# Performance work log

Hardware: AMD Instinct MI355X
Metric: run time of the kernel (lower is better)

## Reference

```python
import jax, jax.numpy as jnp
import numpy as np

T, B, E, H = 2048, 2, 2048, 16
D = E // H  # 128


def setup_inputs() -> dict:
    key = jax.random.key(0)
    ks = jax.random.split(key, 4)
    query = jax.random.normal(ks[0], (T, B, E), dtype=jnp.float32)
    Wqkv = jax.random.normal(ks[1], (3 * E, E), dtype=jnp.float32) * 0.02
    bqkv = jnp.zeros((3 * E,), dtype=jnp.float32)
    Wo = jax.random.normal(ks[2], (E, E), dtype=jnp.float32) * 0.02
    bo = jnp.zeros((E,), dtype=jnp.float32)
    # Llama rotary frequencies: freqs_cis[t, j] = exp(i * t * theta^{-2j/D})
    inv_freq = 1.0 / (10000.0 ** (np.arange(0, D, 2, dtype=np.float32) / D))  # (D/2,)
    angles = np.arange(T, dtype=np.float32)[:, None] * inv_freq[None, :]       # (T, D/2)
    freqs_cos = jnp.asarray(np.cos(angles), dtype=jnp.float32)
    freqs_sin = jnp.asarray(np.sin(angles), dtype=jnp.float32)
    return {"query": query, "Wqkv": Wqkv, "bqkv": bqkv, "Wo": Wo, "bo": bo,
            "freqs_cos": freqs_cos, "freqs_sin": freqs_sin}


def _apply_rope(x, cos, sin):
    # Faithful to metaseq: x is (T, B, E) but view()-ed as (B, T, H, D);
    # jnp.reshape is the same row-major reinterpretation as torch .view().
    xr = x.reshape(B, T, H, D // 2, 2)
    x0, x1 = xr[..., 0], xr[..., 1]
    c = cos[None, :, None, :]  # broadcast over batch and heads, seq_dim=1
    s = sin[None, :, None, :]
    o0 = x0 * c - x1 * s
    o1 = x0 * s + x1 * c
    return jnp.stack([o0, o1], axis=-1).reshape(T, B, E)


def reference(query, Wqkv, bqkv, Wo, bo, freqs_cos, freqs_sin):
    # Combined QKV projection (ColumnParallelLinear, world_size=1), split order (k, v, q)
    kvq = jnp.einsum('tbe,fe->tbf', query, Wqkv) + bqkv  # (T, B, 3E)
    k, v, q = jnp.split(kvq, 3, axis=-1)
    q = _apply_rope(q, freqs_cos, freqs_sin)
    k = _apply_rope(k, freqs_cos, freqs_sin)
    # scaling split as sqrt(head_dim^-0.5) on both q and k (baddbmm path)
    s = jnp.asarray(D, jnp.float32) ** -0.25
    qb = q.reshape(T, B * H, D).swapaxes(0, 1) * s   # (BH, T, D)
    kb = k.reshape(T, B * H, D).swapaxes(0, 1) * s   # (BH, S, D)
    vb = v.reshape(T, B * H, D).swapaxes(0, 1)       # (BH, S, D)
    scores = jnp.einsum('btd,bsd->bts', qb, kb)      # (BH, T, S)
    causal = jnp.tril(jnp.ones((T, T), dtype=bool))  # ScaledUpperTriangMaskedSoftmax
    scores = jnp.where(causal[None, :, :], scores, jnp.finfo(scores.dtype).min)
    probs = jax.nn.softmax(scores, axis=-1)          # dropout p=0 -> identity
    attn = jnp.einsum('bts,bsd->btd', probs, vb)     # (BH, T, D)
    attn = attn.swapaxes(0, 1).reshape(T, B, E)
    # RowParallelLinear with skip_bias_add=True: bias returned separately (not added)
    out = jnp.einsum('tbe,fe->tbf', attn, Wo)
    return out
```

## Files before the change

kernel.cpp:

```cpp
#include <hip/hip_runtime.h>
#include <stdint.h>

typedef unsigned short u16;
typedef __attribute__((ext_vector_type(4))) float f32x4;
typedef __attribute__((ext_vector_type(8))) short bf16x8;
typedef __attribute__((ext_vector_type(8))) u16 u16x8;

#define T_SEQ  2048
#define EMB    2048
#define HD     128
#define NHEAD  16
#define NTOK   4096
#define NE3    6144
#define SCALE  0.29730177875068026f
#define LOG2E  1.44269504088896f

typedef __attribute__((address_space(3))) char* lds_t;
typedef const __attribute__((address_space(1))) char* gl_t;

__device__ __forceinline__ void gld16(const void* g, void* l) {
  __builtin_amdgcn_global_load_lds((gl_t)g, (lds_t)l, 16, 0, 0);
}

__device__ __forceinline__ u16 f2bf(float f) {
  union { float f; uint32_t u; } c; c.f = f;
  uint32_t r = c.u + 0x7fffu + ((c.u >> 16) & 1u);
  return (u16)(r >> 16);
}

__global__ __launch_bounds__(256) void cvt_bf16(const float* __restrict__ in,
                                                u16* __restrict__ out, int n8) {
  int i = blockIdx.x * 256 + threadIdx.x;
  if (i >= n8) return;
  const float4* p = (const float4*)in + (size_t)i * 2;
  float4 a = p[0], b = p[1];
  u16x8 o;
  o[0]=f2bf(a.x); o[1]=f2bf(a.y); o[2]=f2bf(a.z); o[3]=f2bf(a.w);
  o[4]=f2bf(b.x); o[5]=f2bf(b.y); o[6]=f2bf(b.z); o[7]=f2bf(b.w);
  *((u16x8*)out + i) = o;
}


__device__ __forceinline__ bf16x8 rdfrag(const char* slot, int row, int lq) {
  return *(const bf16x8*)(slot + row*64 + ((lq ^ ((row >> 1) & 3)) << 4));
}
__device__ __forceinline__ void stageA(const char* Ag, int K2, int ktb, int ks,
                                       char* slot, int tid) {
  int row = tid >> 2, c = tid & 3;
  gld16(Ag + (size_t)row*K2 + ktb + ks*64 + ((c ^ ((row >> 1) & 3)) << 4),
        slot + tid*16);
}
__device__ __forceinline__ void stageB(const char* Bg, int K2, int ktb, int ks,
                                       char* slot, int j, int tid) {
  int lb = j*8192 + tid*16;
  int row = lb >> 6, c = (lb >> 4) & 3;
  gld16(Bg + (size_t)row*K2 + ktb + ks*64 + ((c ^ ((row >> 1) & 3)) << 4),
        slot + lb);
}

template<int EPI, int NBN>
__global__ __launch_bounds__(512, 2) void gemmP(
    const u16* __restrict__ A, const u16* __restrict__ Bm, int K, int N,
    const float* __restrict__ cosT, const float* __restrict__ sinT,
    const float* __restrict__ bias,
    u16* __restrict__ Qh, u16* __restrict__ Kh, u16* __restrict__ Vt,
    float* __restrict__ Cout)
{
  __shared__ __align__(16) char lds[147456];
  const int tid = threadIdx.x;
  const int lane = tid & 63, w = tid >> 6;
  const int wm = w >> 2, wn = w & 3;
  const int l15 = lane & 15, lq = lane >> 4;

  const int i = blockIdx.x;
  const int r = i >> 8, x = i & 7, s = (i >> 3) & 31;
  const int regionId = r*8 + x;
  const int RM = regionId & 3, RN = regionId >> 2;
  const int bM = RM*8 + (s >> 2);
  const int bN = RN*4 + (s & 3);

  const char* Ag = (const char*)(A + (size_t)bM * 128 * K);
  const char* Bg = (const char*)(Bm + (size_t)bN * 256 * K);
  const int K2 = K * 2;
  const int nT = K >> 6;
  const int nQ = 2*nT;

  #pragma unroll
  for (int q = 0; q < 5; ++q) {
    int kt = (q >> 1) << 7, ks = q & 1;
    stageA(Ag, K2, kt, ks, lds + q*8192, tid);
    stageB(Bg, K2, kt, ks, lds + 49152 + q*16384, 0, tid);
    stageB(Bg, K2, kt, ks, lds + 49152 + q*16384, 1, tid);
  }

  f32x4 acc[4][4] = {};
  int sRd = 0, sWr = 5;

  for (int q = 0; q < nQ; ++q) {
    const int qs = q + 5;
    const int tsc = (qs >> 1) < nT ? (qs >> 1) : nT - 1;
    const int kss = qs & 1;
    const char* Asl = lds + sRd*8192;
    const char* Bsl = lds + 49152 + sRd*16384;
    char* AslS = lds + sWr*8192;
    char* BslS = lds + 49152 + sWr*16384;

    asm volatile("s_waitcnt vmcnt(12)" ::: "memory");
    __builtin_amdgcn_s_barrier();
    __builtin_amdgcn_sched_barrier(0);

    bf16x8 af[4], bf[4];
    #pragma unroll
    for (int j = 0; j < 4; j++) af[j] = rdfrag(Asl, wm*64 + j*16 + l15, lq);
    #pragma unroll
    for (int j = 0; j < 4; j++) bf[j] = rdfrag(Bsl, wn*64 + j*16 + l15, lq);
    stageA(Ag, K2, tsc << 7, kss, AslS, tid);
    stageB(Bg, K2, tsc << 7, kss, BslS, 0, tid);
    stageB(Bg, K2, tsc << 7, kss, BslS, 1, tid);
    asm volatile("s_waitcnt lgkmcnt(0)" ::: "memory");
    __builtin_amdgcn_sched_barrier(0);
    __builtin_amdgcn_s_setprio(1);
    #pragma unroll
    for (int mi = 0; mi < 4; mi++)
      #pragma unroll
      for (int ni = 0; ni < 4; ni++)
        acc[mi][ni] = __builtin_amdgcn_mfma_f32_16x16x32_bf16(af[mi], bf[ni], acc[mi][ni], 0, 0, 0);
    __builtin_amdgcn_s_setprio(0);

    sRd = sRd + 1 < 6 ? sRd + 1 : 0;
    sWr = sWr + 1 < 6 ? sWr + 1 : 0;
  }
  asm volatile("s_waitcnt vmcnt(0)" ::: "memory");

  if (EPI == 0) {
    #pragma unroll
    for (int mi = 0; mi < 4; mi++) {
      int row = bM*128 + wm*64 + mi*16 + lq*4;
      #pragma unroll
      for (int ni = 0; ni < 4; ni++) {
        int col = bN*256 + wn*64 + ni*16 + l15;
        #pragma unroll
        for (int rr = 0; rr < 4; rr++)
          Cout[(size_t)(row + rr) * N + col] = acc[mi][ni][rr];
      }
    }
  } else {
    const int cbase = bN*256 + wn*64;
    const int seg  = cbase >> 11;
    const int head = (cbase >> 7) & 15;
    #pragma unroll
    for (int mi = 0; mi < 4; mi++) {
      #pragma unroll
      for (int ni = 0; ni < 4; ni++) {
        int col = cbase + ni*16 + l15;
        int d = col & 127;
        float bi = bias[col];
        f32x4 v = acc[mi][ni];
        #pragma unroll
        for (int rr = 0; rr < 4; rr++) {
          int n = bM*128 + wm*64 + mi*16 + lq*4 + rr;
          float val = v[rr] + bi;
          int t = n >> 1, b = n & 1;
          int bh = b*NHEAD + head;
          if (seg == 1) {
            Vt[((size_t)bh*HD + d)*T_SEQ + t] = f2bf(val);
          } else {
            float par = __shfl_xor(val, 1);
            int fidx = d >> 1;
            float cs = cosT[(n & (T_SEQ-1))*64 + fidx];
            float sn = sinT[(n & (T_SEQ-1))*64 + fidx];
            val = (d & 1) ? (par*sn + val*cs) : (val*cs - par*sn);
            val *= SCALE;
            u16* dst = (seg == 0) ? Kh : Qh;
            dst[((size_t)bh*T_SEQ + t)*HD + d] = f2bf(val);
          }
        }
      }
    }
  }
}

__global__ __launch_bounds__(256, 4) void attn_fwd(
    const u16* __restrict__ Qh, const u16* __restrict__ Kh,
    const u16* __restrict__ Vt, u16* __restrict__ O)
{
  const int i = blockIdx.x;
  const int kk = i >> 8, c = i & 255;
  const int bh = (c >> 5) + kk * 8;
  const int b5 = c & 31;
  const int qb = (kk & 1) ? (31 - b5) : b5;

  const int tid = threadIdx.x, lane = tid & 63, w = tid >> 6;
  const int l15 = lane & 15, lq = lane >> 4;

  __shared__ u16 Ks[64*128];
  __shared__ u16 Vs[128*64];
  __shared__ char Ps[4][2048];

  const int q0 = qb*64 + w*16;
  bf16x8 qf[4];
  #pragma unroll
  for (int dc = 0; dc < 4; dc++)
    qf[dc] = *(const bf16x8*)(Qh + ((size_t)bh*T_SEQ + q0 + l15)*HD + dc*32 + lq*8);

  f32x4 o[8] = {};
  float m[4], l_[4];
  #pragma unroll
  for (int r = 0; r < 4; r++) { m[r] = -1e30f; l_[r] = 0.f; }

  const int nkb = qb + 1;
  for (int kb = 0; kb < nkb; ++kb) {
    #pragma unroll
    for (int j = 0; j < 4; j++) {
      int lb = tid*16 + j*4096;
      int row = lb >> 8, bir = lb & 255;
      int sb = bir ^ ((row & 7) << 4);
      gld16((const char*)Kh + (((size_t)bh*T_SEQ + kb*64 + row) << 8) + sb,
            (char*)Ks + lb);
    }
    #pragma unroll
    for (int j = 0; j < 4; j++) {
      int lb = tid*16 + j*4096;
      int row = lb >> 7, bir = lb & 127;
      int sb = bir ^ ((row & 7) << 4);
      gld16((const char*)Vt + ((size_t)(bh*HD + row)*T_SEQ)*2 + kb*128 + sb,
            (char*)Vs + lb);
    }
    __syncthreads();

    f32x4 sacc[4];
    #pragma unroll
    for (int nf = 0; nf < 4; nf++) {
      f32x4 z = {};
      sacc[nf] = z;
      #pragma unroll
      for (int dc = 0; dc < 4; dc++) {
        int row = nf*16 + l15;
        int bir = (dc*64 + lq*16) ^ ((row & 7) << 4);
        bf16x8 kf = *(const bf16x8*)((const char*)Ks + row*256 + bir);
        sacc[nf] = __builtin_amdgcn_mfma_f32_16x16x32_bf16(qf[dc], kf, sacc[nf], 0, 0, 0);
      }
    }

    if (kb == qb) {
      #pragma unroll
      for (int nf = 0; nf < 4; nf++)
        #pragma unroll
        for (int r = 0; r < 4; r++) {
          int key = kb*64 + nf*16 + l15;
          int qr  = q0 + lq*4 + r;
          if (key > qr) sacc[nf][r] = -1e30f;
        }
    }

    #pragma unroll
    for (int r = 0; r < 4; r++) {
      float mx = fmaxf(fmaxf(sacc[0][r], sacc[1][r]), fmaxf(sacc[2][r], sacc[3][r]));
      mx = fmaxf(mx, __shfl_xor(mx, 1));
      mx = fmaxf(mx, __shfl_xor(mx, 2));
      mx = fmaxf(mx, __shfl_xor(mx, 4));
      mx = fmaxf(mx, __shfl_xor(mx, 8));
      float newm = fmaxf(m[r], mx);
      float scale = exp2f((m[r] - newm) * LOG2E);
      float sum = 0.f;
      #pragma unroll
      for (int nf = 0; nf < 4; nf++) {
        float p = exp2f((sacc[nf][r] - newm) * LOG2E);
        sacc[nf][r] = p;
        sum += p;
      }
      sum += __shfl_xor(sum, 1);
      sum += __shfl_xor(sum, 2);
      sum += __shfl_xor(sum, 4);
      sum += __shfl_xor(sum, 8);
      l_[r] = l_[r] * scale + sum;
      m[r] = newm;
      #pragma unroll
      for (int nf = 0; nf < 8; nf++) o[nf][r] *= scale;
    }

    #pragma unroll
    for (int nf = 0; nf < 4; nf++)
      #pragma unroll
      for (int r = 0; r < 4; r++) {
        int prow = lq*4 + r;
        int pbyte = prow*128 + ((((nf*16 + l15)*2)) ^ ((prow & 7) << 4));
        *(u16*)(Ps[w] + pbyte) = f2bf(sacc[nf][r]);
      }

    #pragma unroll
    for (int kc = 0; kc < 2; kc++) {
      int pb = (kc*64 + lq*16) ^ ((l15 & 7) << 4);
      bf16x8 pf = *(const bf16x8*)(Ps[w] + l15*128 + pb);
      #pragma unroll
      for (int nf = 0; nf < 8; nf++) {
        int row = nf*16 + l15;
        int bir = (kc*64 + lq*16) ^ ((row & 7) << 4);
        bf16x8 vf = *(const bf16x8*)((const char*)Vs + row*128 + bir);
        o[nf] = __builtin_amdgcn_mfma_f32_16x16x32_bf16(pf, vf, o[nf], 0, 0, 0);
      }
    }
    __syncthreads();
  }

  const int b = bh >> 4, h = bh & 15;
  #pragma unroll
  for (int r = 0; r < 4; r++) {
    float inv = 1.0f / l_[r];
    int t = q0 + lq*4 + r;
    size_t base = ((size_t)(t*2 + b))*EMB + h*HD;
    #pragma unroll
    for (int nf = 0; nf < 8; nf++)
      O[base + nf*16 + l15] = f2bf(o[nf][r] * inv);
  }
}

extern "C" void kernel_launch(void* const* d_in, const int* in_sizes, int n_in,
                              void* d_out, int out_size, void* d_ws, size_t ws_size,
                              hipStream_t stream) {
  const float* query = (const float*)d_in[0];
  const float* Wqkv  = (const float*)d_in[1];
  const float* bqkv  = (const float*)d_in[2];
  const float* Wo    = (const float*)d_in[3];
  const float* fcos  = (const float*)d_in[5];
  const float* fsin  = (const float*)d_in[6];
  float* out = (float*)d_out;
  char* ws = (char*)d_ws;

  u16* WQb = (u16*)(ws + 0);
  u16* WOb = (u16*)(ws + 25165824);
  u16* A1  = (u16*)(ws + 33554432);
  u16* QH  = (u16*)(ws + 50331648);
  u16* KH  = (u16*)(ws + 67108864);
  u16* VT  = (u16*)(ws + 83886080);

  cvt_bf16<<<4096, 256, 0, stream>>>(query, A1, 1048576);
  cvt_bf16<<<6144, 256, 0, stream>>>(Wqkv, WQb, 1572864);
  cvt_bf16<<<2048, 256, 0, stream>>>(Wo,   WOb,  524288);

  gemmP<1, 24><<<768, 512, 0, stream>>>(A1, WQb, 2048, NE3,
                                        fcos, fsin, bqkv, QH, KH, VT, nullptr);

  attn_fwd<<<1024, 256, 0, stream>>>(QH, KH, VT, A1);

  gemmP<0, 8><<<256, 512, 0, stream>>>(A1, WOb, 2048, EMB,
                                       nullptr, nullptr, nullptr,
                                       nullptr, nullptr, nullptr, out);
}
```

Baseline: 340.9 us.

## Restructure projection GEMM to 4 waves with 128x64 per-wave tiles and 3-stage pipeline

The projection GEMMs now launch 256-thread blocks (4 waves) instead of 512, and each wave computes all 128 rows by 64 columns, which doubles the accumulator tile per wave and raises MFMA work per LDS fragment read. The LDS ring shrinks from 6 half-tile stages to 3 stages of 64-wide K slices, halving shared memory per block and allowing more blocks to be resident. The tradeoff is a shallower prefetch depth, more global-to-LDS loads issued per thread, and higher register pressure from 32 accumulators per wave, which could reduce occupancy or latency hiding.

```diff
diff --git a/kernel.cpp b/kernel.cpp
--- a/kernel.cpp
+++ b/kernel.cpp
@@ -44,32 +44,24 @@
 __device__ __forceinline__ bf16x8 rdfrag(const char* slot, int row, int lq) {
   return *(const bf16x8*)(slot + row*64 + ((lq ^ ((row >> 1) & 3)) << 4));
 }
-__device__ __forceinline__ void stageA(const char* Ag, int K2, int ktb, int ks,
-                                       char* slot, int tid) {
-  int row = tid >> 2, c = tid & 3;
-  gld16(Ag + (size_t)row*K2 + ktb + ks*64 + ((c ^ ((row >> 1) & 3)) << 4),
-        slot + tid*16);
-}
-__device__ __forceinline__ void stageB(const char* Bg, int K2, int ktb, int ks,
-                                       char* slot, int j, int tid) {
-  int lb = j*8192 + tid*16;
+__device__ __forceinline__ void stg(const char* g, int K2, int kb,
+                                    char* slot, int j, int tid) {
+  int lb = j*4096 + tid*16;
   int row = lb >> 6, c = (lb >> 4) & 3;
-  gld16(Bg + (size_t)row*K2 + ktb + ks*64 + ((c ^ ((row >> 1) & 3)) << 4),
-        slot + lb);
+  gld16(g + (size_t)row*K2 + kb + ((c ^ ((row >> 1) & 3)) << 4), slot + lb);
 }
 
 template<int EPI, int NBN>
-__global__ __launch_bounds__(512, 2) void gemmP(
+__global__ __launch_bounds__(256, 2) void gemmW(
     const u16* __restrict__ A, const u16* __restrict__ Bm, int K, int N,
     const float* __restrict__ cosT, const float* __restrict__ sinT,
     const float* __restrict__ bias,
     u16* __restrict__ Qh, u16* __restrict__ Kh, u16* __restrict__ Vt,
     float* __restrict__ Cout)
 {
-  __shared__ __align__(16) char lds[147456];
+  __shared__ __align__(16) char lds[73728];
   const int tid = threadIdx.x;
-  const int lane = tid & 63, w = tid >> 6;
-  const int wm = w >> 2, wn = w & 3;
+  const int lane = tid & 63, wn = tid >> 6;
   const int l15 = lane & 15, lq = lane >> 4;
 
   const int i = blockIdx.x;
@@ -82,60 +74,62 @@
   const char* Ag = (const char*)(A + (size_t)bM * 128 * K);
   const char* Bg = (const char*)(Bm + (size_t)bN * 256 * K);
   const int K2 = K * 2;
-  const int nT = K >> 6;
-  const int nQ = 2*nT;
+  const int nQ = K >> 5;
 
   #pragma unroll
-  for (int q = 0; q < 5; ++q) {
-    int kt = (q >> 1) << 7, ks = q & 1;
-    stageA(Ag, K2, kt, ks, lds + q*8192, tid);
-    stageB(Bg, K2, kt, ks, lds + 49152 + q*16384, 0, tid);
-    stageB(Bg, K2, kt, ks, lds + 49152 + q*16384, 1, tid);
-  }
-
-  f32x4 acc[4][4] = {};
-  int sRd = 0, sWr = 5;
+  for (int q = 0; q < 2; ++q) {
+    stg(Ag, K2, q*64, lds + q*8192, 0, tid);
+    stg(Ag, K2, q*64, lds + q*8192, 1, tid);
+    stg(Bg, K2, q*64, lds + 24576 + q*16384, 0, tid);
+    stg(Bg, K2, q*64, lds + 24576 + q*16384, 1, tid);
+    stg(Bg, K2, q*64, lds + 24576 + q*16384, 2, tid);
+    stg(Bg, K2, q*64, lds + 24576 + q*16384, 3, tid);
+  }
+
+  f32x4 acc[8][4] = {};
+  int sRd = 0, sWr = 2;
 
   for (int q = 0; q < nQ; ++q) {
-    const int qs = q + 5;
-    const int tsc = (qs >> 1) < nT ? (qs >> 1) : nT - 1;
-    const int kss = qs & 1;
+    const int qs = q + 2 < nQ ? q + 2 : nQ - 1;
     const char* Asl = lds + sRd*8192;
-    const char* Bsl = lds + 49152 + sRd*16384;
+    const char* Bsl = lds + 24576 + sRd*16384;
     char* AslS = lds + sWr*8192;
-    char* BslS = lds + 49152 + sWr*16384;
-
-    asm volatile("s_waitcnt vmcnt(12)" ::: "memory");
+    char* BslS = lds + 24576 + sWr*16384;
+
+    asm volatile("s_waitcnt vmcnt(6)" ::: "memory");
     __builtin_amdgcn_s_barrier();
     __builtin_amdgcn_sched_barrier(0);
 
-    bf16x8 af[4], bf[4];
-    #pragma unroll
-    for (int j = 0; j < 4; j++) af[j] = rdfrag(Asl, wm*64 + j*16 + l15, lq);
+    bf16x8 af[8], bf[4];
+    #pragma unroll
+    for (int j = 0; j < 8; j++) af[j] = rdfrag(Asl, j*16 + l15, lq);
     #pragma unroll
     for (int j = 0; j < 4; j++) bf[j] = rdfrag(Bsl, wn*64 + j*16 + l15, lq);
-    stageA(Ag, K2, tsc << 7, kss, AslS, tid);
-    stageB(Bg, K2, tsc << 7, kss, BslS, 0, tid);
-    stageB(Bg, K2, tsc << 7, kss, BslS, 1, tid);
+    stg(Ag, K2, qs*64, AslS, 0, tid);
+    stg(Ag, K2, qs*64, AslS, 1, tid);
+    stg(Bg, K2, qs*64, BslS, 0, tid);
+    stg(Bg, K2, qs*64, BslS, 1, tid);
+    stg(Bg, K2, qs*64, BslS, 2, tid);
+    stg(Bg, K2, qs*64, BslS, 3, tid);
     asm volatile("s_waitcnt lgkmcnt(0)" ::: "memory");
     __builtin_amdgcn_sched_barrier(0);
     __builtin_amdgcn_s_setprio(1);
     #pragma unroll
-    for (int mi = 0; mi < 4; mi++)
+    for (int mi = 0; mi < 8; mi++)
       #pragma unroll
       for (int ni = 0; ni < 4; ni++)
         acc[mi][ni] = __builtin_amdgcn_mfma_f32_16x16x32_bf16(af[mi], bf[ni], acc[mi][ni], 0, 0, 0);
     __builtin_amdgcn_s_setprio(0);
 
-    sRd = sRd + 1 < 6 ? sRd + 1 : 0;
-    sWr = sWr + 1 < 6 ? sWr + 1 : 0;
+    sRd = sRd + 1 < 3 ? sRd + 1 : 0;
+    sWr = sWr + 1 < 3 ? sWr + 1 : 0;
   }
   asm volatile("s_waitcnt vmcnt(0)" ::: "memory");
 
   if (EPI == 0) {
     #pragma unroll
-    for (int mi = 0; mi < 4; mi++) {
-      int row = bM*128 + wm*64 + mi*16 + lq*4;
+    for (int mi = 0; mi < 8; mi++) {
+      int row = bM*128 + mi*16 + lq*4;
       #pragma unroll
       for (int ni = 0; ni < 4; ni++) {
         int col = bN*256 + wn*64 + ni*16 + l15;
@@ -149,7 +143,7 @@
     const int seg  = cbase >> 11;
     const int head = (cbase >> 7) & 15;
     #pragma unroll
-    for (int mi = 0; mi < 4; mi++) {
+    for (int mi = 0; mi < 8; mi++) {
       #pragma unroll
       for (int ni = 0; ni < 4; ni++) {
         int col = cbase + ni*16 + l15;
@@ -158,7 +152,7 @@
         f32x4 v = acc[mi][ni];
         #pragma unroll
         for (int rr = 0; rr < 4; rr++) {
-          int n = bM*128 + wm*64 + mi*16 + lq*4 + rr;
+          int n = bM*128 + mi*16 + lq*4 + rr;
           float val = v[rr] + bi;
           int t = n >> 1, b = n & 1;
           int bh = b*NHEAD + head;
@@ -338,12 +332,12 @@
   cvt_bf16<<<6144, 256, 0, stream>>>(Wqkv, WQb, 1572864);
   cvt_bf16<<<2048, 256, 0, stream>>>(Wo,   WOb,  524288);
 
-  gemmP<1, 24><<<768, 512, 0, stream>>>(A1, WQb, 2048, NE3,
+  gemmW<1, 24><<<768, 256, 0, stream>>>(A1, WQb, 2048, NE3,
                                         fcos, fsin, bqkv, QH, KH, VT, nullptr);
 
   attn_fwd<<<1024, 256, 0, stream>>>(QH, KH, VT, A1);
 
-  gemmP<0, 8><<<256, 512, 0, stream>>>(A1, WOb, 2048, EMB,
+  gemmW<0, 8><<<256, 256, 0, stream>>>(A1, WOb, 2048, EMB,
                                        nullptr, nullptr, nullptr,
                                        nullptr, nullptr, nullptr, out);
 }
```

After: 345.6 us. Within noise of the previous version (+1.4%).
